# Performance work log

Measured on AMD Instinct MI355X. Metric: run time of the kernel, lower is better.

The kernel has to match this reference:

```python
import jax, jax.numpy as jnp
import numpy as np
import math
from jax import lax

# cfg['MODEL'] constants
MU = 0.1          # FISTA step size
LMBD = 0.1        # LAMBDA[0], sparsity weight
N_DICT = 1        # EXPANSION_FACTOR
N_STEPS = 6       # NUM_LAYERS (FISTA iterations)
K = 3             # kernel_size
PAD = 1           # padding
STRIDE = 1        # stride (POOLING=False, stride passed to conv)
DN = ('NCHW', 'OIHW', 'NCHW')


def _conv(x, w):
    # F.conv2d(x, w, stride=1, padding=PAD)
    return lax.conv_general_dilated(x, w, (STRIDE, STRIDE), [(PAD, PAD), (PAD, PAD)], dimension_numbers=DN)


def _conv_t(y, w):
    # F.conv_transpose2d(y, w, stride=1, padding=PAD) == conv2d with flipped, in/out-swapped kernel, pad K-1-PAD
    wt = jnp.transpose(jnp.flip(w, (-1, -2)), (1, 0, 2, 3))  # [Cin, Cout, K, K]
    p = K - 1 - PAD
    return lax.conv_general_dilated(y, wt, (1, 1), [(p, p), (p, p)], dimension_numbers=DN)


def _shrink(z, thr):
    # non_negative=True soft-threshold: relu(z - thr)
    return jax.nn.relu(z - thr)


def setup_inputs() -> dict:
    key = jax.random.key(0)
    k1, k2 = jax.random.split(key)
    x = jax.random.normal(k1, (16, 64, 56, 56), dtype=jnp.float32)
    # dictionary weight [out_channels, in_channels*n_dict, K, K], kaiming-ish scale
    W = jax.random.normal(k2, (128, 64 * N_DICT, K, K), dtype=jnp.float32) * 0.05
    return {"x": x, "W": W}


def reference(x, W):
    # w_norm: each output filter normalized to unit Frobenius norm
    Wn = W / jnp.sqrt(jnp.sum(W * W, axis=(1, 2, 3), keepdims=True) + 1e-12)
    thr = MU * LMBD
    xr = jnp.tile(x, (1, N_DICT, 1, 1)) if N_DICT > 1 else x

    # FISTA iteration 0: c = shrink(mu * D^T x)
    c = _shrink(MU * _conv(xr, Wn), thr)
    y = c
    c_prev = c
    t = 1.0
    for _ in range(N_STEPS - 1):
        r = xr - _conv_t(y, Wn)                       # residual x - D c
        c_new = _shrink(y + MU * _conv(r, Wn), thr)   # gradient step + shrink
        t_next = (1.0 + math.sqrt(1.0 + 4.0 * t * t)) / 2.0
        y = c_new + ((t - 1.0) / t_next) * (c_new - c_prev)  # momentum
        c_prev = c_new
        t = t_next
    # POOLING=False -> DictConv2d returns the sparse code directly
    return c_prev
```

## Files before the change

### kernel.cpp

```cpp
#include <hip/hip_runtime.h>
#include <hip/hip_bf16.h>
#include <math.h>

typedef __attribute__((ext_vector_type(8))) short short8;
typedef __attribute__((ext_vector_type(4))) float f32x4;

#define MU_  0.1f
#define THR_ 0.01f
#define ZB_  204

static __device__ inline short f2bf(float f) {
    __hip_bfloat16 h = __float2bfloat16(f);
    return *reinterpret_cast<short*>(&h);
}
static __device__ inline float bf2f(unsigned short u) {
    unsigned int x = ((unsigned int)u) << 16;
    return __builtin_bit_cast(float, x);
}

__global__ __launch_bounds__(256) void prep_kernel(
    const float* __restrict__ x, const float* __restrict__ W,
    short* __restrict__ Rp, short* __restrict__ Yp,
    short* __restrict__ Xp, short* __restrict__ Wf2, short* __restrict__ Wt2) {
    __shared__ float lx[64 * 57];
    const int bid = blockIdx.x, tid = threadIdx.x;
    if (bid < ZB_) {
        int gid = bid * 256 + tid;
        const short8 z = {0, 0, 0, 0, 0, 0, 0, 0};
        if (gid < 17408) {
            int ridx = gid / 544, off = gid - ridx * 544;
            int n = ridx >> 1, row = (ridx & 1) * 57;
            ((short8*)(Rp + ((size_t)(n * 58 + row) * 68) * 64))[off] = z;
        } else {
            int g2 = gid - 17408;
            int ridx = g2 / 1088, off = g2 - ridx * 1088;
            int n = ridx >> 1, row = (ridx & 1) * 57;
            ((short8*)(Yp + ((size_t)(n * 58 + row) * 68) * 128))[off] = z;
        }
    } else if (bid < ZB_ + 32) {
        int co = (bid - ZB_) * 4 + (tid >> 6);
        int ci = tid & 63;
        const float* wp = W + (co * 64 + ci) * 9;
        float v[9]; float s = 0.f;
#pragma unroll
        for (int t = 0; t < 9; ++t) { v[t] = wp[t]; s += v[t] * v[t]; }
#pragma unroll
        for (int off = 32; off; off >>= 1) s += __shfl_xor(s, off, 64);
        float inv = 1.0f / sqrtf(s + 1e-12f);
#pragma unroll
        for (int t = 0; t < 9; ++t) {
            Wf2[((t * 8 + (ci >> 3)) * 128 + co) * 8 + (ci & 7)] = f2bf(v[t] * inv);
            Wt2[((t * 16 + (co >> 3)) * 64 + ci) * 8 + (co & 7)] = f2bf(v[8 - t] * inv);
        }
    } else {
        int pb = bid - ZB_ - 32;
        int row = pb % 58, n = pb / 58;
        short* dst = Xp + ((size_t)(n * 58 + row) * 68) * 64;
        if (row >= 1 && row <= 56) {
            int h = row - 1;
            for (int j = tid; j < 64 * 56; j += 256) {
                int ci = j / 56, w = j - ci * 56;
                lx[ci * 57 + w] = x[((size_t)(n * 64 + ci)) * 3136 + h * 56 + w];
            }
            __syncthreads();
            for (int j = tid; j < 68 * 64; j += 256) {
                int s = j >> 6, ci = j & 63;
                float val = (s >= 2 && s < 58) ? lx[ci * 57 + (s - 2)] : 0.f;
                dst[(s << 6) + (ci ^ ((s & 7) << 3))] = f2bf(val);
            }
        } else {
            for (int j = tid; j < 68 * 64; j += 256) dst[j] = 0;
        }
    }
}

static __device__ __forceinline__ void zero_lds_pads4(short* smem, int tid) {
    const short8 z = {0, 0, 0, 0, 0, 0, 0, 0};
    for (int i = tid; i < 384; i += 256) {
        int sr = i >> 3, w = i & 7;
        int row = sr / 12, sl = sr - row * 12;
        int s = (sl < 2) ? sl : sl + 56;
        *(short8*)(smem + (row * 68 + s) * 72 + w * 8) = z;
    }
}

__global__ __launch_bounds__(256, 2) void conv_fwd(
    const short* __restrict__ inp,
    const short* __restrict__ Wf2,
    short* __restrict__ Yp,
    short* __restrict__ Cp,
    float* __restrict__ outp, int mode, float beta) {
    __shared__ __align__(16) short smem[38016];
    const int bid = blockIdx.x, tid = threadIdx.x;
    const int sid0 = (bid & 7) * 112 + (bid >> 3) * 2;
    const int n = sid0 / 56, r0 = sid0 - n * 56 + 1;
    zero_lds_pads4(smem, tid);
    {
        const short8* src = (const short8*)(inp + ((size_t)(n * 58 + (r0 - 1)) * 68) * 64);
        for (int j = tid; j < 1792; j += 256) {
            int sr = j >> 3, w = j & 7;
            int row = sr / 56, s = sr - row * 56 + 2;
            *(short8*)(smem + (row * 68 + s) * 72 + w * 8) = src[(row * 68 + s) * 8 + w];
        }
    }
    const int lane = tid & 63, ct = tid >> 6, quad = lane >> 4, l15 = lane & 15;
    const int cog = ct & 1, pxg = ct >> 1;
    size_t prow[2];
    prow[0] = ((size_t)(n * 58 + r0) * 68) * 128;
    prow[1] = prow[0] + 68 * 128;

    short8 yold8[2][2], cold8[2][2];
    int pvv[2], pg[2]; bool pok[2];
#pragma unroll
    for (int k = 0; k < 2; ++k) {
        int item = tid + k * 256;
        pok[k] = item < 448;
        pvv[k] = item >> 3; pg[k] = item & 7;
        if (mode != 0 && pok[k]) {
            int s = pvv[k] + 2;
            int xo = 8 * (pg[k] ^ (s & 7));
#pragma unroll
            for (int rw = 0; rw < 2; ++rw) {
                size_t off = prow[rw] + (size_t)s * 128 + xo;
                yold8[rw][k] = *(const short8*)(Yp + off);
                if (mode == 1) cold8[rw][k] = *(const short8*)(Cp + off);
            }
        }
    }
    __syncthreads();

    f32x4 acc[2][2][4];
#pragma unroll
    for (int rw = 0; rw < 2; ++rw)
#pragma unroll
        for (int pt = 0; pt < 2; ++pt)
#pragma unroll
            for (int cot = 0; cot < 4; ++cot) acc[rw][pt][cot] = (f32x4){0.f, 0.f, 0.f, 0.f};

#pragma unroll
    for (int f = 0; f < 18; ++f) {
        const int t = f >> 1, half = f & 1;
        const int dh = t / 3, dw = t % 3;
        const int u = l15 + dw + 1;
        const int phys = (half * 4 + quad) ^ (u & 7);
        short8 areg[4];
#pragma unroll
        for (int cot = 0; cot < 4; ++cot) {
            const int co = cog * 64 + cot * 16 + l15;
            areg[cot] = *(const short8*)(Wf2 +
                ((size_t)((t * 8 + half * 4 + quad) * 128 + co)) * 8);
        }
#pragma unroll
        for (int rw = 0; rw < 2; ++rw) {
#pragma unroll
            for (int pt = 0; pt < 2; ++pt) {
                const int pti = pxg * 2 + pt;
                const short8 bv = *(const short8*)(smem +
                    ((dh + rw) * 68 + pti * 16 + u) * 72 + phys * 8);
#pragma unroll
                for (int cot = 0; cot < 4; ++cot)
                    acc[rw][pt][cot] = __builtin_amdgcn_mfma_f32_16x16x32_bf16(areg[cot], bv, acc[rw][pt][cot], 0, 0, 0);
            }
        }
    }

    short* tbase = smem + 19584;
    const int h0 = r0 - 1;
#pragma unroll
    for (int hh = 0; hh < 2; ++hh) {
        if (mode != 0) {
#pragma unroll
            for (int rw = 0; rw < 2; ++rw) {
                short* tb_y = tbase + rw * 9216;
                short* tb_c = tb_y + 4608;
#pragma unroll
                for (int k = 0; k < 2; ++k) if (pok[k]) {
                    int o = pvv[k] * 72 + 8 * (pg[k] ^ (pvv[k] & 3));
                    *(short8*)(tb_y + o) = yold8[rw][k];
                    if (mode == 1) *(short8*)(tb_c + o) = cold8[rw][k];
                }
            }
        }
        __syncthreads();
        if (hh == 0 && mode != 0) {
#pragma unroll
            for (int k = 0; k < 2; ++k) if (pok[k]) {
                int s = pvv[k] + 2;
                int xo = 8 * ((pg[k] + 8) ^ (s & 7));
#pragma unroll
                for (int rw = 0; rw < 2; ++rw) {
                    size_t off = prow[rw] + (size_t)s * 128 + xo;
                    yold8[rw][k] = *(const short8*)(Yp + off);
                    if (mode == 1) cold8[rw][k] = *(const short8*)(Cp + off);
                }
            }
        }
        if (cog == hh) {
#pragma unroll
            for (int rw = 0; rw < 2; ++rw) {
                short* tb_y = tbase + rw * 9216;
                short* tb_c = tb_y + 4608;
#pragma unroll
                for (int pt = 0; pt < 2; ++pt) {
                    const int px = pxg * 32 + pt * 16 + l15;
#pragma unroll
                    for (int cot = 0; cot < 4; ++cot) {
#pragma unroll
                        for (int reg = 0; reg < 4; ++reg) {
                            const int lch = cot * 16 + quad * 4 + reg;
                            const int slot = px * 72 + (lch ^ ((px & 3) << 3));
                            const float a = acc[rw][pt][cot][reg];
                            if (mode == 0) {
                                float c = fmaxf(MU_ * a - THR_, 0.f);
                                short cb16 = f2bf(c);
                                tb_y[slot] = cb16;
                                tb_c[slot] = cb16;
                            } else if (mode == 1) {
                                float yold = bf2f((unsigned short)tb_y[slot]);
                                float cold = bf2f((unsigned short)tb_c[slot]);
                                float c = fmaxf(yold + MU_ * a - THR_, 0.f);
                                tb_y[slot] = f2bf(c + beta * (c - cold));
                                tb_c[slot] = f2bf(c);
                            } else {
                                if (px < 56) {
                                    float yold = bf2f((unsigned short)tb_y[slot]);
                                    float c = fmaxf(yold + MU_ * a - THR_, 0.f);
                                    outp[((size_t)(n * 128 + hh * 64 + lch)) * 3136 + (h0 + rw) * 56 + px] = c;
                                }
                            }
                        }
                    }
                }
            }
        }
        if (mode != 2) {
            __syncthreads();
            for (int item = tid; item < 448; item += 256) {
                int vv = item >> 3, g = item & 7;
                int so = vv * 72 + 8 * (g ^ (vv & 3));
                int s = vv + 2;
                int xo = 8 * ((g + 8 * hh) ^ (s & 7));
#pragma unroll
                for (int rw = 0; rw < 2; ++rw) {
                    short* tb_y = tbase + rw * 9216;
                    short8 yv = *(const short8*)(tb_y + so);
                    short8 cv = *(const short8*)(tb_y + 4608 + so);
                    size_t off = prow[rw] + (size_t)s * 128 + xo;
                    *(short8*)(Yp + off) = yv;
                    *(short8*)(Cp + off) = cv;
                }
            }
        }
        if (hh == 0) __syncthreads();
    }
}

__global__ __launch_bounds__(256, 2) void conv_t(
    const short* __restrict__ Ypb,
    const short* __restrict__ Wt2,
    const short* __restrict__ Xp,
    short* __restrict__ Rp) {
    __shared__ __align__(16) short smem[28800];
    const int bid = blockIdx.x, tid = threadIdx.x;
    const int sid0 = (bid & 7) * 112 + (bid >> 3) * 2;
    const int n = sid0 / 56, r0 = sid0 - n * 56 + 1;
    const int lane = tid & 63, ct = tid >> 6, quad = lane >> 4, l15 = lane & 15;
    const short8* src = (const short8*)(Ypb + ((size_t)(n * 58 + (r0 - 1)) * 68) * 128);
    size_t prowX[2];
    prowX[0] = ((size_t)(n * 58 + r0) * 68) * 64;
    prowX[1] = prowX[0] + 68 * 64;

    short8 xold8[2][2];
    int pvv[2], pg[2]; bool pok[2];
#pragma unroll
    for (int k = 0; k < 2; ++k) {
        int item = tid + k * 256;
        pok[k] = item < 448;
        pvv[k] = item >> 3; pg[k] = item & 7;
        if (pok[k]) {
            int s = pvv[k] + 2;
            int xo = 8 * (pg[k] ^ (s & 7));
#pragma unroll
            for (int rw = 0; rw < 2; ++rw)
                xold8[rw][k] = *(const short8*)(Xp + prowX[rw] + (size_t)s * 64 + xo);
        }
    }

    zero_lds_pads4(smem, tid);
    for (int j = tid; j < 1792; j += 256) {
        int sr = j >> 3, w = j & 7;
        int row = sr / 56, s = sr - row * 56 + 2;
        *(short8*)(smem + (row * 68 + s) * 72 + w * 8) = src[(row * 68 + s) * 16 + w];
    }

    f32x4 acc[2][4];
#pragma unroll
    for (int rw = 0; rw < 2; ++rw)
#pragma unroll
        for (int cit = 0; cit < 4; ++cit) acc[rw][cit] = (f32x4){0.f, 0.f, 0.f, 0.f};

    __syncthreads();

    short8 pf[7];
#pragma unroll
    for (int k = 0; k < 7; ++k) {
        int j = tid + k * 256;
        if (j < 1792) {
            int sr = j >> 3, w = j & 7;
            int row = sr / 56, s = sr - row * 56 + 2;
            pf[k] = src[(row * 68 + s) * 16 + 8 + w];
        }
    }

#pragma unroll
    for (int p = 0; p < 2; ++p) {
        if (p) {
            __syncthreads();
#pragma unroll
            for (int k = 0; k < 7; ++k) {
                int j = tid + k * 256;
                if (j < 1792) {
                    int sr = j >> 3, w = j & 7;
                    int row = sr / 56, s = sr - row * 56 + 2;
                    *(short8*)(smem + (row * 68 + s) * 72 + w * 8) = pf[k];
                }
            }
            __syncthreads();
        }
#pragma unroll
        for (int f = 0; f < 18; ++f) {
            const int t = f >> 1, sh = f & 1;
            const int dh = t / 3, dw = t % 3;
            const int u = l15 + dw + 1;
            const int phys = (sh * 4 + quad) ^ (u & 7);
            short8 areg[4];
#pragma unroll
            for (int cit = 0; cit < 4; ++cit) {
                const int ci = cit * 16 + l15;
                areg[cit] = *(const short8*)(Wt2 +
                    ((size_t)((t * 16 + (p * 2 + sh) * 4 + quad) * 64 + ci)) * 8);
            }
#pragma unroll
            for (int rw = 0; rw < 2; ++rw) {
                const short8 bv = *(const short8*)(smem +
                    ((dh + rw) * 68 + ct * 16 + u) * 72 + phys * 8);
#pragma unroll
                for (int cit = 0; cit < 4; ++cit)
                    acc[rw][cit] = __builtin_amdgcn_mfma_f32_16x16x32_bf16(areg[cit], bv, acc[rw][cit], 0, 0, 0);
            }
        }
    }

    short* tbase = smem + 19584;
#pragma unroll
    for (int rw = 0; rw < 2; ++rw) {
#pragma unroll
        for (int k = 0; k < 2; ++k) if (pok[k]) {
            *(short8*)(tbase + rw * 4608 + pvv[k] * 72 + 8 * (pg[k] ^ (pvv[k] & 3))) = xold8[rw][k];
        }
    }
    __syncthreads();
    {
        const int px = ct * 16 + l15;
#pragma unroll
        for (int rw = 0; rw < 2; ++rw) {
            short* tb = tbase + rw * 4608;
#pragma unroll
            for (int cit = 0; cit < 4; ++cit) {
#pragma unroll
                for (int reg = 0; reg < 4; ++reg) {
                    const int cir = cit * 16 + quad * 4 + reg;
                    const int slot = px * 72 + (cir ^ ((px & 3) << 3));
                    float xo = bf2f((unsigned short)tb[slot]);
                    tb[slot] = f2bf(xo - acc[rw][cit][reg]);
                }
            }
        }
    }
    __syncthreads();
    for (int item = tid; item < 448; item += 256) {
        int vv = item >> 3, g = item & 7;
        int so = vv * 72 + 8 * (g ^ (vv & 3));
        int s = vv + 2;
        int xo = 8 * (g ^ (s & 7));
#pragma unroll
        for (int rw = 0; rw < 2; ++rw) {
            short8 val = *(const short8*)(tbase + rw * 4608 + so);
            *(short8*)(Rp + prowX[rw] + (size_t)s * 64 + xo) = val;
        }
    }
}

extern "C" void kernel_launch(void* const* d_in, const int* in_sizes, int n_in,
                              void* d_out, int out_size, void* d_ws, size_t ws_size,
                              hipStream_t stream) {
    const float* x = (const float*)d_in[0];
    const float* W = (const float*)d_in[1];
    float* out = (float*)d_out;

    const size_t XPN = (size_t)16 * 58 * 68 * 64;
    const size_t YPN = 2 * XPN;
    short* Xp = (short*)d_ws;
    short* Rp = Xp + XPN;
    short* Yp = Rp + XPN;
    short* Cp = Yp + YPN;
    short* Wf2 = Cp + YPN;
    short* Wt2 = Wf2 + 73728;

    const int prep_blocks = ZB_ + 32 + 58 * 16;
    hipLaunchKernelGGL(prep_kernel, dim3(prep_blocks), dim3(256), 0, stream,
                       x, W, Rp, Yp, Xp, Wf2, Wt2);

    dim3 b(256, 1, 1);
    hipLaunchKernelGGL(conv_fwd, dim3(448), b, 0, stream, Xp, Wf2, Yp, Cp,
                       (float*)nullptr, 0, 0.f);
    double t = 1.0;
    for (int it = 1; it <= 5; ++it) {
        hipLaunchKernelGGL(conv_t, dim3(448), b, 0, stream, Yp, Wt2, Xp, Rp);
        double tn = (1.0 + sqrt(1.0 + 4.0 * t * t)) / 2.0;
        float beta = (float)((t - 1.0) / tn);
        hipLaunchKernelGGL(conv_fwd, dim3(448), b, 0, stream, Rp, Wf2, Yp, Cp,
                           (it == 5) ? out : (float*)nullptr, (it == 5) ? 2 : 1,
                           beta);
        t = tn;
    }
}
```

Baseline: 344.3 us.

## Fuse input packing and pad zeroing into first forward conv launch

Splits weight normalization into its own small kernel, then merges the x-to-bf16 packing, border zeroing and the first forward convolution into one launch. The first conv blocks now read x straight from global memory, transpose it through LDS and convert it in place, so they no longer wait for a separate prep kernel to write Xp. The cost is redundant conversion: each conv block converts 4 rows of x, and separate blocks still write Xp for later iterations. The fused conv blocks also carry heavier prologues with extra syncs.

Measured after the change: 356.4 us. 3.5% more time.

```diff
diff --git a/kernel.cpp b/kernel.cpp
--- a/kernel.cpp
+++ b/kernel.cpp
@@ -7,7 +7,6 @@
 
 #define MU_  0.1f
 #define THR_ 0.01f
-#define ZB_  204
 
 static __device__ inline short f2bf(float f) {
     __hip_bfloat16 h = __float2bfloat16(f);
@@ -18,59 +17,22 @@
     return __builtin_bit_cast(float, x);
 }
 
-__global__ __launch_bounds__(256) void prep_kernel(
-    const float* __restrict__ x, const float* __restrict__ W,
-    short* __restrict__ Rp, short* __restrict__ Yp,
-    short* __restrict__ Xp, short* __restrict__ Wf2, short* __restrict__ Wt2) {
-    __shared__ float lx[64 * 57];
-    const int bid = blockIdx.x, tid = threadIdx.x;
-    if (bid < ZB_) {
-        int gid = bid * 256 + tid;
-        const short8 z = {0, 0, 0, 0, 0, 0, 0, 0};
-        if (gid < 17408) {
-            int ridx = gid / 544, off = gid - ridx * 544;
-            int n = ridx >> 1, row = (ridx & 1) * 57;
-            ((short8*)(Rp + ((size_t)(n * 58 + row) * 68) * 64))[off] = z;
-        } else {
-            int g2 = gid - 17408;
-            int ridx = g2 / 1088, off = g2 - ridx * 1088;
-            int n = ridx >> 1, row = (ridx & 1) * 57;
-            ((short8*)(Yp + ((size_t)(n * 58 + row) * 68) * 128))[off] = z;
-        }
-    } else if (bid < ZB_ + 32) {
-        int co = (bid - ZB_) * 4 + (tid >> 6);
-        int ci = tid & 63;
-        const float* wp = W + (co * 64 + ci) * 9;
-        float v[9]; float s = 0.f;
-#pragma unroll
-        for (int t = 0; t < 9; ++t) { v[t] = wp[t]; s += v[t] * v[t]; }
-#pragma unroll
-        for (int off = 32; off; off >>= 1) s += __shfl_xor(s, off, 64);
-        float inv = 1.0f / sqrtf(s + 1e-12f);
-#pragma unroll
-        for (int t = 0; t < 9; ++t) {
-            Wf2[((t * 8 + (ci >> 3)) * 128 + co) * 8 + (ci & 7)] = f2bf(v[t] * inv);
-            Wt2[((t * 16 + (co >> 3)) * 64 + ci) * 8 + (co & 7)] = f2bf(v[8 - t] * inv);
-        }
-    } else {
-        int pb = bid - ZB_ - 32;
-        int row = pb % 58, n = pb / 58;
-        short* dst = Xp + ((size_t)(n * 58 + row) * 68) * 64;
-        if (row >= 1 && row <= 56) {
-            int h = row - 1;
-            for (int j = tid; j < 64 * 56; j += 256) {
-                int ci = j / 56, w = j - ci * 56;
-                lx[ci * 57 + w] = x[((size_t)(n * 64 + ci)) * 3136 + h * 56 + w];
-            }
-            __syncthreads();
-            for (int j = tid; j < 68 * 64; j += 256) {
-                int s = j >> 6, ci = j & 63;
-                float val = (s >= 2 && s < 58) ? lx[ci * 57 + (s - 2)] : 0.f;
-                dst[(s << 6) + (ci ^ ((s & 7) << 3))] = f2bf(val);
-            }
-        } else {
-            for (int j = tid; j < 68 * 64; j += 256) dst[j] = 0;
-        }
+__global__ __launch_bounds__(256) void wnorm_kernel(
+    const float* __restrict__ W,
+    short* __restrict__ Wf2, short* __restrict__ Wt2) {
+    int co = blockIdx.x * 4 + (threadIdx.x >> 6);
+    int ci = threadIdx.x & 63;
+    const float* wp = W + (co * 64 + ci) * 9;
+    float v[9]; float s = 0.f;
+#pragma unroll
+    for (int t = 0; t < 9; ++t) { v[t] = wp[t]; s += v[t] * v[t]; }
+#pragma unroll
+    for (int off = 32; off; off >>= 1) s += __shfl_xor(s, off, 64);
+    float inv = 1.0f / sqrtf(s + 1e-12f);
+#pragma unroll
+    for (int t = 0; t < 9; ++t) {
+        Wf2[((t * 8 + (ci >> 3)) * 128 + co) * 8 + (ci & 7)] = f2bf(v[t] * inv);
+        Wt2[((t * 16 + (co >> 3)) * 64 + ci) * 8 + (co & 7)] = f2bf(v[8 - t] * inv);
     }
 }
 
@@ -84,25 +46,10 @@
     }
 }
 
-__global__ __launch_bounds__(256, 2) void conv_fwd(
-    const short* __restrict__ inp,
-    const short* __restrict__ Wf2,
-    short* __restrict__ Yp,
-    short* __restrict__ Cp,
-    float* __restrict__ outp, int mode, float beta) {
-    __shared__ __align__(16) short smem[38016];
-    const int bid = blockIdx.x, tid = threadIdx.x;
-    const int sid0 = (bid & 7) * 112 + (bid >> 3) * 2;
-    const int n = sid0 / 56, r0 = sid0 - n * 56 + 1;
-    zero_lds_pads4(smem, tid);
-    {
-        const short8* src = (const short8*)(inp + ((size_t)(n * 58 + (r0 - 1)) * 68) * 64);
-        for (int j = tid; j < 1792; j += 256) {
-            int sr = j >> 3, w = j & 7;
-            int row = sr / 56, s = sr - row * 56 + 2;
-            *(short8*)(smem + (row * 68 + s) * 72 + w * 8) = src[(row * 68 + s) * 8 + w];
-        }
-    }
+static __device__ __forceinline__ void fwd_from_lds(
+    short* smem, int tid, int n, int r0,
+    const short* __restrict__ Wf2, short* __restrict__ Yp,
+    short* __restrict__ Cp, float* __restrict__ outp, int mode, float beta) {
     const int lane = tid & 63, ct = tid >> 6, quad = lane >> 4, l15 = lane & 15;
     const int cog = ct & 1, pxg = ct >> 1;
     size_t prow[2];
@@ -255,6 +202,101 @@
     }
 }
 
+__global__ __launch_bounds__(256, 2) void prep_main(
+    const float* __restrict__ x, const short* __restrict__ Wf2,
+    short* __restrict__ Rp, short* __restrict__ Yp, short* __restrict__ Cp,
+    short* __restrict__ Xp) {
+    __shared__ __align__(16) short smem[38016];
+    const int bid = blockIdx.x, tid = threadIdx.x;
+    if (bid < 448) {
+        const int sid0 = (bid & 7) * 112 + (bid >> 3) * 2;
+        const int n = sid0 / 56, r0 = sid0 - n * 56 + 1;
+        zero_lds_pads4(smem, tid);
+        float* lx = (float*)(smem + 19584);
+        for (int rr = 0; rr < 4; ++rr) {
+            const int h = r0 - 2 + rr;
+            if (h >= 0 && h < 56) {
+                for (int j = tid; j < 64 * 56; j += 256) {
+                    int ci = j / 56, w = j - ci * 56;
+                    lx[ci * 57 + w] = x[((size_t)(n * 64 + ci)) * 3136 + h * 56 + w];
+                }
+                __syncthreads();
+                for (int j = tid; j < 448; j += 256) {
+                    int s = 2 + (j >> 3), w = j & 7;
+                    int cibase = (w ^ (s & 7)) * 8;
+                    short* dst = smem + (rr * 68 + s) * 72 + w * 8;
+#pragma unroll
+                    for (int e = 0; e < 8; ++e)
+                        dst[e] = f2bf(lx[(cibase + e) * 57 + (s - 2)]);
+                }
+                __syncthreads();
+            } else {
+                const short8 z = {0, 0, 0, 0, 0, 0, 0, 0};
+                for (int j = tid; j < 448; j += 256) {
+                    int s = 2 + (j >> 3), w = j & 7;
+                    *(short8*)(smem + (rr * 68 + s) * 72 + w * 8) = z;
+                }
+            }
+        }
+        fwd_from_lds(smem, tid, n, r0, Wf2, Yp, Cp, (float*)nullptr, 0, 0.f);
+    } else if (bid < 652) {
+        int gid = (bid - 448) * 256 + tid;
+        const short8 z = {0, 0, 0, 0, 0, 0, 0, 0};
+        if (gid < 17408) {
+            int ridx = gid / 544, off = gid - ridx * 544;
+            int n = ridx >> 1, row = (ridx & 1) * 57;
+            ((short8*)(Rp + ((size_t)(n * 58 + row) * 68) * 64))[off] = z;
+        } else {
+            int g2 = gid - 17408;
+            int ridx = g2 / 1088, off = g2 - ridx * 1088;
+            int n = ridx >> 1, row = (ridx & 1) * 57;
+            ((short8*)(Yp + ((size_t)(n * 58 + row) * 68) * 128))[off] = z;
+        }
+    } else {
+        int pb = bid - 652;
+        int row = pb % 58, n = pb / 58;
+        float* lx = (float*)smem;
+        short* dst = Xp + ((size_t)(n * 58 + row) * 68) * 64;
+        if (row >= 1 && row <= 56) {
+            int h = row - 1;
+            for (int j = tid; j < 64 * 56; j += 256) {
+                int ci = j / 56, w = j - ci * 56;
+                lx[ci * 57 + w] = x[((size_t)(n * 64 + ci)) * 3136 + h * 56 + w];
+            }
+            __syncthreads();
+            for (int j = tid; j < 68 * 64; j += 256) {
+                int s = j >> 6, ci = j & 63;
+                float val = (s >= 2 && s < 58) ? lx[ci * 57 + (s - 2)] : 0.f;
+                dst[(s << 6) + (ci ^ ((s & 7) << 3))] = f2bf(val);
+            }
+        } else {
+            for (int j = tid; j < 68 * 64; j += 256) dst[j] = 0;
+        }
+    }
+}
+
+__global__ __launch_bounds__(256, 2) void conv_fwd(
+    const short* __restrict__ inp,
+    const short* __restrict__ Wf2,
+    short* __restrict__ Yp,
+    short* __restrict__ Cp,
+    float* __restrict__ outp, int mode, float beta) {
+    __shared__ __align__(16) short smem[38016];
+    const int bid = blockIdx.x, tid = threadIdx.x;
+    const int sid0 = (bid & 7) * 112 + (bid >> 3) * 2;
+    const int n = sid0 / 56, r0 = sid0 - n * 56 + 1;
+    zero_lds_pads4(smem, tid);
+    {
+        const short8* src = (const short8*)(inp + ((size_t)(n * 58 + (r0 - 1)) * 68) * 64);
+        for (int j = tid; j < 1792; j += 256) {
+            int sr = j >> 3, w = j & 7;
+            int row = sr / 56, s = sr - row * 56 + 2;
+            *(short8*)(smem + (row * 68 + s) * 72 + w * 8) = src[(row * 68 + s) * 8 + w];
+        }
+    }
+    fwd_from_lds(smem, tid, n, r0, Wf2, Yp, Cp, outp, mode, beta);
+}
+
 __global__ __launch_bounds__(256, 2) void conv_t(
     const short* __restrict__ Ypb,
     const short* __restrict__ Wt2,
@@ -407,13 +449,10 @@
     short* Wf2 = Cp + YPN;
     short* Wt2 = Wf2 + 73728;
 
-    const int prep_blocks = ZB_ + 32 + 58 * 16;
-    hipLaunchKernelGGL(prep_kernel, dim3(prep_blocks), dim3(256), 0, stream,
-                       x, W, Rp, Yp, Xp, Wf2, Wt2);
-
     dim3 b(256, 1, 1);
-    hipLaunchKernelGGL(conv_fwd, dim3(448), b, 0, stream, Xp, Wf2, Yp, Cp,
-                       (float*)nullptr, 0, 0.f);
+    hipLaunchKernelGGL(wnorm_kernel, dim3(32), b, 0, stream, W, Wf2, Wt2);
+    hipLaunchKernelGGL(prep_main, dim3(1580), b, 0, stream,
+                       x, Wf2, Rp, Yp, Cp, Xp);
     double t = 1.0;
     for (int it = 1; it <= 5; ++it) {
         hipLaunchKernelGGL(conv_t, dim3(448), b, 0, stream, Yp, Wt2, Xp, Rp);
```
